# Kernel optimization log

Hardware: AMD Instinct MI355X
Metric: run time of the kernel (lower is better)

Reference implementation:

```python
import jax, jax.numpy as jnp
import numpy as np

EMBED_DIM = 1024
HEAD_DIM = 64


def setup_inputs() -> dict:
    key = jax.random.key(0)
    ks = jax.random.split(key, 7)
    s_in = EMBED_DIM ** -0.5  # torch Linear default init scale
    x = jax.random.normal(ks[0], (4, 4096, EMBED_DIM), dtype=jnp.float32)
    Wk = jax.random.uniform(ks[1], (HEAD_DIM, EMBED_DIM), jnp.float32, -s_in, s_in)
    bk = jax.random.uniform(ks[2], (HEAD_DIM,), jnp.float32, -s_in, s_in)
    Wq = jax.random.uniform(ks[3], (HEAD_DIM, EMBED_DIM), jnp.float32, -s_in, s_in)
    bq = jax.random.uniform(ks[4], (HEAD_DIM,), jnp.float32, -s_in, s_in)
    Wv = jax.random.uniform(ks[5], (HEAD_DIM, EMBED_DIM), jnp.float32, -s_in, s_in)
    bv = jax.random.uniform(ks[6], (HEAD_DIM,), jnp.float32, -s_in, s_in)
    return {"x": x, "Wq": Wq, "bq": bq, "Wk": Wk, "bk": bk, "Wv": Wv, "bv": bv}


def reference(x, Wq, bq, Wk, bk, Wv, bv):
    # torch Linear: y = x @ W.T + b
    q = jnp.einsum('btc,dc->btd', x, Wq) + bq  # [B,T,D]
    k = jnp.einsum('btc,dc->btd', x, Wk) + bk
    v = jnp.einsum('btc,dc->btd', x, Wv) + bv
    scale = HEAD_DIM ** -0.5
    # NOTE: original divides by scale (multiplies by sqrt(head_dim)) -- faithful
    scores = jnp.einsum('btd,bsd->bts', q, k) / scale  # [B,T,T]
    attn_weights = jax.nn.softmax(scores, axis=-1)
    return jnp.einsum('bts,bsd->btd', attn_weights, v)
```

## Files before the change

kernel.cpp:

```cpp
#include <hip/hip_runtime.h>

#define BATCH 4
#define SEQ   4096
#define CDIM  1024
#define DDIM  64
#define NROW  (BATCH * SEQ)
#define NSPL  8
#define KS    4
#define SEG   (NROW * DDIM)

typedef _Float16 f16;
typedef _Float16 f16x8 __attribute__((ext_vector_type(8)));
typedef _Float16 f16x4 __attribute__((ext_vector_type(4)));
typedef __fp16   h16x2 __attribute__((ext_vector_type(2)));
typedef float    f32x4 __attribute__((ext_vector_type(4)));

#define MFMA32(a, b, c) __builtin_amdgcn_mfma_f32_16x16x32_f16((a), (b), (c), 0, 0, 0)
#define MFMA16(a, b, c) __builtin_amdgcn_mfma_f32_16x16x16f16((a), (b), (c), 0, 0, 0)

#define GLDS(g, l)                                                            \
  __builtin_amdgcn_global_load_lds((const __attribute__((address_space(1))) void*)(g), \
                                   (__attribute__((address_space(3))) void*)(l), 16, 0, 0)

#define QSCALE 11.5415603f

__device__ inline f16x8 cvt8(f32x4 a, f32x4 b) {
  h16x2 p0 = __builtin_amdgcn_cvt_pkrtz(a[0], a[1]);
  h16x2 p1 = __builtin_amdgcn_cvt_pkrtz(a[2], a[3]);
  h16x2 p2 = __builtin_amdgcn_cvt_pkrtz(b[0], b[1]);
  h16x2 p3 = __builtin_amdgcn_cvt_pkrtz(b[2], b[3]);
  f16x8 r;
  r[0] = p0[0]; r[1] = p0[1]; r[2] = p1[0]; r[3] = p1[1];
  r[4] = p2[0]; r[5] = p2[1]; r[6] = p3[0]; r[7] = p3[1];
  return r;
}

__device__ inline f16x4 cvt4(float a, float b, float c, float d) {
  h16x2 lo = __builtin_amdgcn_cvt_pkrtz(a, b);
  h16x2 hi = __builtin_amdgcn_cvt_pkrtz(c, d);
  f16x4 r;
  r[0] = lo[0]; r[1] = lo[1]; r[2] = hi[0]; r[3] = hi[1];
  return r;
}

__global__ __launch_bounds__(256) void prep_w_kernel(const float* __restrict__ Wq,
                                                     const float* __restrict__ Wk,
                                                     const float* __restrict__ Wv,
                                                     f16* __restrict__ wf2) {
  const int t = blockIdx.x * 256 + threadIdx.x;
  const int lane = t & 63;
  const int s = t >> 6;
  const int mt = s % 12, ck = s / 12;
  const int mat = mt >> 2, tile = mt & 3;
  const int n = lane & 15, quad = lane >> 4;
  const float* W = (mat == 0) ? Wq : (mat == 1) ? Wk : Wv;
  const float* src = W + (size_t)(tile * 16 + n) * CDIM + ck * 32 + quad * 8;
  const f32x4 a = *(const f32x4*)src;
  const f32x4 b = *(const f32x4*)(src + 4);
  *(f16x8*)(wf2 + (size_t)t * 8) = cvt8(a, b);
}

__global__ __launch_bounds__(256, 4) void proj_kernel(const float* __restrict__ x,
                                                      const f16* __restrict__ wf2,
                                                      f16* __restrict__ ppart) {
  __shared__ __attribute__((aligned(16))) char smem[2][20480];
  const int tid = threadIdx.x, lane = tid & 63, w = tid >> 6;
  const int n = lane & 15, quad = lane >> 4;
  const int rw = w & 1, wc = w >> 1;
  const int rowblk = blockIdx.x >> 2, split = blockIdx.x & 3;
  const int rowbase = rowblk * 64;

  const float* xsrc[2];
#pragma unroll
  for (int j = 0; j < 2; ++j) {
    const int i = 2 * w + j;
    xsrc[j] = x + (size_t)(rowbase + i * 8 + (lane >> 3)) * CDIM + split * 256 + (lane & 7) * 4;
  }
  const f16* wsrc[3];
#pragma unroll
  for (int j = 0; j < 3; ++j) {
    const int mt = 3 * w + j;
    wsrc[j] = wf2 + (size_t)(split * 96 + mt) * 512 + lane * 8;
  }

  f32x4 acc[2][6];
#pragma unroll
  for (int rt = 0; rt < 2; ++rt)
#pragma unroll
    for (int i = 0; i < 6; ++i) acc[rt][i] = (f32x4){0.f, 0.f, 0.f, 0.f};

  auto issue = [&](int ck, int b) {
    char* base = &smem[b][0];
#pragma unroll
    for (int j = 0; j < 2; ++j)
      GLDS(xsrc[j] + ck * 32, base + (2 * w + j) * 1024);
#pragma unroll
    for (int j = 0; j < 3; ++j)
      GLDS(wsrc[j] + (size_t)ck * 6144, base + 8192 + (3 * w + j) * 1024);
  };

  issue(0, 0);
  for (int ck = 0; ck < 8; ++ck) {
    const int b = ck & 1;
    __syncthreads();
    if (ck + 1 < 8) issue(ck + 1, b ^ 1);
    const char* base = &smem[b][0];
    f16x8 a[2];
#pragma unroll
    for (int rt = 0; rt < 2; ++rt) {
      const int i = rw * 4 + rt * 2 + (n >> 3);
      const float* xp = (const float*)(base + i * 1024 + (n & 7) * 128 + quad * 32);
      a[rt] = cvt8(*(const f32x4*)xp, *(const f32x4*)(xp + 4));
    }
#pragma unroll
    for (int i2 = 0; i2 < 6; ++i2) {
      const f16x8 bf = *(const f16x8*)(base + 8192 + (wc * 6 + i2) * 1024 + lane * 16);
      acc[0][i2] = MFMA32(a[0], bf, acc[0][i2]);
      acc[1][i2] = MFMA32(a[1], bf, acc[1][i2]);
    }
  }

#pragma unroll
  for (int i2 = 0; i2 < 6; ++i2) {
    const int mt = wc * 6 + i2;
    const int mat = mt >> 2, tile = mt & 3;
    const int d = tile * 16 + n;
    f16* seg = ppart + ((size_t)mat * KS + split) * SEG;
#pragma unroll
    for (int rt = 0; rt < 2; ++rt) {
      const int r0 = rowbase + rw * 32 + rt * 16 + quad * 4;
      const f32x4 aa = acc[rt][i2];
      if (mat == 0) {
#pragma unroll
        for (int r = 0; r < 4; ++r)
          seg[(size_t)(r0 + r) * DDIM + d] = (f16)aa[r];
      } else if (mat == 1) {
#pragma unroll
        for (int r = 0; r < 4; ++r) {
          const int t = r0 + r;
          const int col = ((((d >> 3) ^ (t & 7)) << 3) | (d & 7));
          seg[(size_t)t * DDIM + col] = (f16)aa[r];
        }
      } else {
        const int bb = r0 >> 12;
        const int tl = r0 & (SEQ - 1);
        const int ck2 = tl >> 6;
        const int bsw = (((tl & 63) >> 2) ^ n) << 2;
        *(f16x4*)(seg + ((size_t)(bb * 64 + ck2) * 64 + d) * 64 + bsw) =
            cvt4(aa[0], aa[1], aa[2], aa[3]);
      }
    }
  }
}

__global__ __launch_bounds__(256) void combine_proj_kernel(const f16* __restrict__ ppart,
                                                           const float* __restrict__ bq,
                                                           const float* __restrict__ bk,
                                                           const float* __restrict__ bv,
                                                           f16* __restrict__ qs,
                                                           f16* __restrict__ ks,
                                                           f16* __restrict__ vc) {
  const int seg = blockIdx.x / 512;
  const int tix = (blockIdx.x - seg * 512) * 256 + threadIdx.x;
  const size_t base = (size_t)tix * 8;
  const f16* pp = ppart + (size_t)seg * KS * SEG + base;

  float s[8];
#pragma unroll
  for (int j = 0; j < 8; ++j) s[j] = 0.f;
#pragma unroll
  for (int sp = 0; sp < KS; ++sp) {
    const f16x8 v = *(const f16x8*)(pp + (size_t)sp * SEG);
#pragma unroll
    for (int j = 0; j < 8; ++j) s[j] += (float)v[j];
  }

  f16x8 o;
  if (seg == 0) {
    const int d0 = (int)(base & 63);
#pragma unroll
    for (int j = 0; j < 8; ++j) o[j] = (f16)((s[j] + bq[d0 + j]) * QSCALE);
    *(f16x8*)(qs + base) = o;
  } else if (seg == 1) {
    const int t = (int)(base >> 6);
    const int d0 = (((int)(base & 63) >> 3) ^ (t & 7)) << 3;
#pragma unroll
    for (int j = 0; j < 8; ++j) o[j] = (f16)(s[j] + bk[d0 + j]);
    *(f16x8*)(ks + base) = o;
  } else {
    const float b = bv[(int)(base >> 6) & 63];
#pragma unroll
    for (int j = 0; j < 8; ++j) o[j] = (f16)(s[j] + b);
    *(f16x8*)(vc + base) = o;
  }
}

template <int NSPLIT>
__global__ __launch_bounds__(256, 4) void attn_kernel(const f16* __restrict__ qs,
                                                      const f16* __restrict__ ks,
                                                      const f16* __restrict__ vc,
                                                      float* __restrict__ outp,
                                                      f16* __restrict__ pacc,
                                                      float* __restrict__ pm,
                                                      float* __restrict__ pl) {
  __shared__ __attribute__((aligned(16))) f16 lk[2][4096];
  __shared__ __attribute__((aligned(16))) f16 lv[2][4096];
  const int tid = threadIdx.x, lane = tid & 63, w = tid >> 6;
  const int n = lane & 15, quad = lane >> 4;
  const int split = blockIdx.x % NSPLIT;
  const int rowblk = blockIdx.x / NSPLIT;
  const int row0 = rowblk * 128 + w * 32;
  const int bb = row0 >> 12;
  const int kbase = split * (SEQ / NSPLIT);
  const int kc0 = kbase >> 6;
  const int NC = SEQ / NSPLIT / 64;

  const f16* ksb = ks + (size_t)bb * SEQ * DDIM;
  const f16* vcb = vc + (size_t)bb * 64 * 4096;

  auto issue = [&](int c, int buf) {
#pragma unroll
    for (int i = 0; i < 2; ++i) {
      const int id = 2 * w + i;
      GLDS(ksb + (size_t)(kbase + c * 64) * 64 + id * 512 + lane * 8, &lk[buf][id * 512]);
      GLDS(vcb + (size_t)(kc0 + c) * 4096 + id * 512 + lane * 8, &lv[buf][id * 512]);
    }
  };

  f16x8 qf[2][2];
#pragma unroll
  for (int g = 0; g < 2; ++g)
#pragma unroll
    for (int hh = 0; hh < 2; ++hh)
      qf[g][hh] = *(const f16x8*)(qs + (size_t)(row0 + g * 16 + n) * DDIM + hh * 32 + quad * 8);

  const int kswz = (quad ^ (n & 7)) << 3;
  int vswz[4];
#pragma unroll
  for (int st = 0; st < 4; ++st) vswz[st] = ((((st << 2) | quad) ^ n) << 2);

  f32x4 acc[2][4];
  float m[2] = {-1e30f, -1e30f}, ll[2] = {0.f, 0.f};
#pragma unroll
  for (int g = 0; g < 2; ++g)
#pragma unroll
    for (int t = 0; t < 4; ++t) acc[g][t] = (f32x4){0.f, 0.f, 0.f, 0.f};

  issue(0, 0);
  for (int c = 0; c < NC; ++c) {
    const int b = c & 1;
    __syncthreads();
    if (c + 1 < NC) issue(c + 1, b ^ 1);

    f32x4 s[2][4];
#pragma unroll
    for (int st = 0; st < 4; ++st) {
      const f16* lkr = &lk[b][(st * 16 + n) * 64];
      const f16x8 klo = *(const f16x8*)(lkr + kswz);
      const f16x8 khi = *(const f16x8*)(lkr + (kswz ^ 32));
#pragma unroll
      for (int g = 0; g < 2; ++g) {
        f32x4 z = (f32x4){0.f, 0.f, 0.f, 0.f};
        z = MFMA32(klo, qf[g][0], z);
        s[g][st] = MFMA32(khi, qf[g][1], z);
      }
    }

    f16x4 pq[2][4];
#pragma unroll
    for (int g = 0; g < 2; ++g) {
      f32x4 mx;
#pragma unroll
      for (int r = 0; r < 4; ++r)
        mx[r] = fmaxf(fmaxf(s[g][0][r], s[g][1][r]), fmaxf(s[g][2][r], s[g][3][r]));
      float mloc = fmaxf(fmaxf(mx[0], mx[1]), fmaxf(mx[2], mx[3]));
      mloc = fmaxf(mloc, __shfl_xor(mloc, 16));
      mloc = fmaxf(mloc, __shfl_xor(mloc, 32));
      const float mnew = fmaxf(m[g], mloc);
      const float alpha = __builtin_amdgcn_exp2f(m[g] - mnew);
      m[g] = mnew;
      float psum = 0.f;
#pragma unroll
      for (int st = 0; st < 4; ++st) {
        f32x4 p;
#pragma unroll
        for (int r = 0; r < 4; ++r) p[r] = __builtin_amdgcn_exp2f(s[g][st][r] - mnew);
        psum += (p[0] + p[1]) + (p[2] + p[3]);
        pq[g][st] = cvt4(p[0], p[1], p[2], p[3]);
      }
      ll[g] = ll[g] * alpha + psum;
#pragma unroll
      for (int t = 0; t < 4; ++t) acc[g][t] *= alpha;
    }

#pragma unroll
    for (int dt = 0; dt < 4; ++dt) {
      const f16* lvr = &lv[b][(dt * 16 + n) * 64];
#pragma unroll
      for (int st = 0; st < 4; ++st) {
        const f16x4 va = *(const f16x4*)(lvr + vswz[st]);
        acc[0][dt] = MFMA16(va, pq[0][st], acc[0][dt]);
        acc[1][dt] = MFMA16(va, pq[1][st], acc[1][dt]);
      }
    }
  }

  float lred[2];
#pragma unroll
  for (int g = 0; g < 2; ++g) {
    float l = ll[g];
    l += __shfl_xor(l, 16);
    l += __shfl_xor(l, 32);
    lred[g] = l;
  }

  if (NSPLIT == 1) {
#pragma unroll
    for (int g = 0; g < 2; ++g) {
      const float inv = 1.0f / lred[g];
      const int q = row0 + g * 16 + n;
#pragma unroll
      for (int t = 0; t < 4; ++t) {
        f32x4 o = acc[g][t];
#pragma unroll
        for (int r = 0; r < 4; ++r) o[r] *= inv;
        *(f32x4*)(outp + (size_t)q * DDIM + t * 16 + quad * 4) = o;
      }
    }
  } else {
#pragma unroll
    for (int g = 0; g < 2; ++g) {
      const int q = row0 + g * 16 + n;
#pragma unroll
      for (int t = 0; t < 4; ++t)
        *(f16x4*)(pacc + ((size_t)split * NROW + q) * DDIM + t * 16 + quad * 4) =
            cvt4(acc[g][t][0], acc[g][t][1], acc[g][t][2], acc[g][t][3]);
      if (quad == 0) {
        pm[split * NROW + q] = m[g];
        pl[split * NROW + q] = lred[g];
      }
    }
  }
}

template <int NSPLIT>
__global__ __launch_bounds__(256) void combine_kernel(const f16* __restrict__ pacc,
                                                      const float* __restrict__ pm,
                                                      const float* __restrict__ pl,
                                                      float* __restrict__ out) {
  const int idx = blockIdx.x * 256 + threadIdx.x;
  const int row = idx >> 4;
  const int c = (idx & 15) * 4;
  float mm = pm[row];
#pragma unroll
  for (int s = 1; s < NSPLIT; ++s) mm = fmaxf(mm, pm[s * NROW + row]);
  float L = 0.f;
  f32x4 o = (f32x4){0.f, 0.f, 0.f, 0.f};
#pragma unroll
  for (int s = 0; s < NSPLIT; ++s) {
    const float e = __builtin_amdgcn_exp2f(pm[s * NROW + row] - mm);
    L += pl[s * NROW + row] * e;
    const f16x4 a = *(const f16x4*)(pacc + ((size_t)s * NROW + row) * DDIM + c);
#pragma unroll
    for (int j = 0; j < 4; ++j) o[j] += (float)a[j] * e;
  }
  const float inv = 1.0f / L;
#pragma unroll
  for (int j = 0; j < 4; ++j) o[j] *= inv;
  *(f32x4*)(out + (size_t)row * DDIM + c) = o;
}

extern "C" void kernel_launch(void* const* d_in, const int* in_sizes, int n_in,
                              void* d_out, int out_size, void* d_ws, size_t ws_size,
                              hipStream_t stream) {
  const float* x  = (const float*)d_in[0];
  const float* Wq = (const float*)d_in[1];
  const float* bq = (const float*)d_in[2];
  const float* Wk = (const float*)d_in[3];
  const float* bk = (const float*)d_in[4];
  const float* Wv = (const float*)d_in[5];
  const float* bv = (const float*)d_in[6];
  float* out = (float*)d_out;

  f16* wf2 = (f16*)d_ws;
  f16* qs = wf2 + 3 * 65536;
  f16* ks = qs + (size_t)SEG;
  f16* vc = ks + (size_t)SEG;
  f16* ppart = vc + (size_t)SEG;
  f16* pacc = ppart + (size_t)3 * KS * SEG;
  float* pm = (float*)(pacc + (size_t)NSPL * SEG);
  float* pl = pm + (size_t)NSPL * NROW;
  const size_t need = (size_t)((char*)(pl + (size_t)NSPL * NROW) - (char*)d_ws);

  prep_w_kernel<<<dim3(96), dim3(256), 0, stream>>>(Wq, Wk, Wv, wf2);
  proj_kernel<<<dim3(256 * KS), dim3(256), 0, stream>>>(x, wf2, ppart);
  combine_proj_kernel<<<dim3(1536), dim3(256), 0, stream>>>(ppart, bq, bk, bv, qs, ks, vc);

  if (ws_size >= need) {
    attn_kernel<NSPL><<<dim3(128 * NSPL), dim3(256), 0, stream>>>(qs, ks, vc, nullptr, pacc, pm, pl);
    combine_kernel<NSPL><<<dim3(NROW * 16 / 256), dim3(256), 0, stream>>>(pacc, pm, pl, out);
  } else {
    attn_kernel<1><<<dim3(128), dim3(256), 0, stream>>>(qs, ks, vc, out, nullptr, nullptr, nullptr);
  }
}
```

Before: 158.1 us.

## Drop split-K in projection and fuse bias/combine into proj kernel

The projection kernel no longer splits the 1024-wide reduction into four partial fp16 buffers that a separate combine kernel sums. Each 512-thread block now handles 32 rows over the full reduction in 32 double-buffered steps and adds the bias and Q scale directly before writing Q, K and V. The x tile in shared memory uses an XOR swizzle to avoid bank conflicts. This removes one kernel launch and the write and reread of the partial buffers, but leaves fewer blocks and a longer serial reduction loop per block.

```diff
diff --git a/kernel.cpp b/kernel.cpp
--- a/kernel.cpp
+++ b/kernel.cpp
@@ -6,7 +6,6 @@
 #define DDIM  64
 #define NROW  (BATCH * SEQ)
 #define NSPL  8
-#define KS    4
 #define SEG   (NROW * DDIM)
 
 typedef _Float16 f16;
@@ -60,138 +59,101 @@
   *(f16x8*)(wf2 + (size_t)t * 8) = cvt8(a, b);
 }
 
-__global__ __launch_bounds__(256, 4) void proj_kernel(const float* __restrict__ x,
+__global__ __launch_bounds__(512, 4) void proj_kernel(const float* __restrict__ x,
                                                       const f16* __restrict__ wf2,
-                                                      f16* __restrict__ ppart) {
-  __shared__ __attribute__((aligned(16))) char smem[2][20480];
+                                                      const float* __restrict__ bq,
+                                                      const float* __restrict__ bk,
+                                                      const float* __restrict__ bv,
+                                                      f16* __restrict__ qs,
+                                                      f16* __restrict__ ks,
+                                                      f16* __restrict__ vc) {
+  __shared__ __attribute__((aligned(16))) char smem[2][16384];
   const int tid = threadIdx.x, lane = tid & 63, w = tid >> 6;
   const int n = lane & 15, quad = lane >> 4;
-  const int rw = w & 1, wc = w >> 1;
-  const int rowblk = blockIdx.x >> 2, split = blockIdx.x & 3;
-  const int rowbase = rowblk * 64;
-
-  const float* xsrc[2];
-#pragma unroll
-  for (int j = 0; j < 2; ++j) {
-    const int i = 2 * w + j;
-    xsrc[j] = x + (size_t)(rowbase + i * 8 + (lane >> 3)) * CDIM + split * 256 + (lane & 7) * 4;
-  }
-  const f16* wsrc[3];
-#pragma unroll
-  for (int j = 0; j < 3; ++j) {
-    const int mt = 3 * w + j;
-    wsrc[j] = wf2 + (size_t)(split * 96 + mt) * 512 + lane * 8;
-  }
-
-  f32x4 acc[2][6];
-#pragma unroll
-  for (int rt = 0; rt < 2; ++rt)
-#pragma unroll
-    for (int i = 0; i < 6; ++i) acc[rt][i] = (f32x4){0.f, 0.f, 0.f, 0.f};
+  const int rowbase = blockIdx.x * 32;
+
+  const float* xsrc[2] = {nullptr, nullptr};
+  const f16* wsrc[2] = {nullptr, nullptr};
+  int xdst[2] = {0, 0}, wdst[2] = {0, 0};
+  if (w < 2) {
+#pragma unroll
+    for (int j = 0; j < 2; ++j) {
+      const int i = 2 * w + j;
+      xsrc[j] = x + (size_t)(rowbase + i * 8 + (lane >> 3)) * CDIM +
+                (((lane & 7) ^ ((lane >> 3) & 7)) * 4);
+      xdst[j] = i * 1024;
+    }
+  } else {
+#pragma unroll
+    for (int j = 0; j < 2; ++j) {
+      const int mt = 2 * (w - 2) + j;
+      wsrc[j] = wf2 + (size_t)mt * 512 + lane * 8;
+      wdst[j] = 4096 + mt * 1024;
+    }
+  }
 
   auto issue = [&](int ck, int b) {
     char* base = &smem[b][0];
-#pragma unroll
-    for (int j = 0; j < 2; ++j)
-      GLDS(xsrc[j] + ck * 32, base + (2 * w + j) * 1024);
-#pragma unroll
-    for (int j = 0; j < 3; ++j)
-      GLDS(wsrc[j] + (size_t)ck * 6144, base + 8192 + (3 * w + j) * 1024);
+    if (w < 2) {
+#pragma unroll
+      for (int j = 0; j < 2; ++j) GLDS(xsrc[j] + ck * 32, base + xdst[j]);
+    } else {
+#pragma unroll
+      for (int j = 0; j < 2; ++j) GLDS(wsrc[j] + (size_t)ck * 6144, base + wdst[j]);
+    }
   };
 
+  const int rt = w >> 2, mtb = 3 * (w & 3);
+  f32x4 acc[3];
+#pragma unroll
+  for (int i = 0; i < 3; ++i) acc[i] = (f32x4){0.f, 0.f, 0.f, 0.f};
+
   issue(0, 0);
-  for (int ck = 0; ck < 8; ++ck) {
+  for (int ck = 0; ck < 32; ++ck) {
     const int b = ck & 1;
     __syncthreads();
-    if (ck + 1 < 8) issue(ck + 1, b ^ 1);
+    if (ck + 1 < 32) issue(ck + 1, b ^ 1);
     const char* base = &smem[b][0];
-    f16x8 a[2];
-#pragma unroll
-    for (int rt = 0; rt < 2; ++rt) {
-      const int i = rw * 4 + rt * 2 + (n >> 3);
-      const float* xp = (const float*)(base + i * 1024 + (n & 7) * 128 + quad * 32);
-      a[rt] = cvt8(*(const f32x4*)xp, *(const f32x4*)(xp + 4));
-    }
-#pragma unroll
-    for (int i2 = 0; i2 < 6; ++i2) {
-      const f16x8 bf = *(const f16x8*)(base + 8192 + (wc * 6 + i2) * 1024 + lane * 16);
-      acc[0][i2] = MFMA32(a[0], bf, acc[0][i2]);
-      acc[1][i2] = MFMA32(a[1], bf, acc[1][i2]);
-    }
-  }
-
-#pragma unroll
-  for (int i2 = 0; i2 < 6; ++i2) {
-    const int mt = wc * 6 + i2;
+    const char* xb = base + (rt * 16 + n) * 128;
+    const f32x4 xa = *(const f32x4*)(xb + ((((quad << 1) ^ (n & 7)) << 4)));
+    const f32x4 xc = *(const f32x4*)(xb + (((((quad << 1) | 1) ^ (n & 7)) << 4)));
+    const f16x8 a = cvt8(xa, xc);
+#pragma unroll
+    for (int i2 = 0; i2 < 3; ++i2) {
+      const f16x8 bf = *(const f16x8*)(base + 4096 + (mtb + i2) * 1024 + lane * 16);
+      acc[i2] = MFMA32(a, bf, acc[i2]);
+    }
+  }
+
+  const int r0 = rowbase + rt * 16 + quad * 4;
+#pragma unroll
+  for (int i2 = 0; i2 < 3; ++i2) {
+    const int mt = mtb + i2;
     const int mat = mt >> 2, tile = mt & 3;
     const int d = tile * 16 + n;
-    f16* seg = ppart + ((size_t)mat * KS + split) * SEG;
-#pragma unroll
-    for (int rt = 0; rt < 2; ++rt) {
-      const int r0 = rowbase + rw * 32 + rt * 16 + quad * 4;
-      const f32x4 aa = acc[rt][i2];
-      if (mat == 0) {
-#pragma unroll
-        for (int r = 0; r < 4; ++r)
-          seg[(size_t)(r0 + r) * DDIM + d] = (f16)aa[r];
-      } else if (mat == 1) {
-#pragma unroll
-        for (int r = 0; r < 4; ++r) {
-          const int t = r0 + r;
-          const int col = ((((d >> 3) ^ (t & 7)) << 3) | (d & 7));
-          seg[(size_t)t * DDIM + col] = (f16)aa[r];
-        }
-      } else {
-        const int bb = r0 >> 12;
-        const int tl = r0 & (SEQ - 1);
-        const int ck2 = tl >> 6;
-        const int bsw = (((tl & 63) >> 2) ^ n) << 2;
-        *(f16x4*)(seg + ((size_t)(bb * 64 + ck2) * 64 + d) * 64 + bsw) =
-            cvt4(aa[0], aa[1], aa[2], aa[3]);
-      }
-    }
-  }
-}
-
-__global__ __launch_bounds__(256) void combine_proj_kernel(const f16* __restrict__ ppart,
-                                                           const float* __restrict__ bq,
-                                                           const float* __restrict__ bk,
-                                                           const float* __restrict__ bv,
-                                                           f16* __restrict__ qs,
-                                                           f16* __restrict__ ks,
-                                                           f16* __restrict__ vc) {
-  const int seg = blockIdx.x / 512;
-  const int tix = (blockIdx.x - seg * 512) * 256 + threadIdx.x;
-  const size_t base = (size_t)tix * 8;
-  const f16* pp = ppart + (size_t)seg * KS * SEG + base;
-
-  float s[8];
-#pragma unroll
-  for (int j = 0; j < 8; ++j) s[j] = 0.f;
-#pragma unroll
-  for (int sp = 0; sp < KS; ++sp) {
-    const f16x8 v = *(const f16x8*)(pp + (size_t)sp * SEG);
-#pragma unroll
-    for (int j = 0; j < 8; ++j) s[j] += (float)v[j];
-  }
-
-  f16x8 o;
-  if (seg == 0) {
-    const int d0 = (int)(base & 63);
-#pragma unroll
-    for (int j = 0; j < 8; ++j) o[j] = (f16)((s[j] + bq[d0 + j]) * QSCALE);
-    *(f16x8*)(qs + base) = o;
-  } else if (seg == 1) {
-    const int t = (int)(base >> 6);
-    const int d0 = (((int)(base & 63) >> 3) ^ (t & 7)) << 3;
-#pragma unroll
-    for (int j = 0; j < 8; ++j) o[j] = (f16)(s[j] + bk[d0 + j]);
-    *(f16x8*)(ks + base) = o;
-  } else {
-    const float b = bv[(int)(base >> 6) & 63];
-#pragma unroll
-    for (int j = 0; j < 8; ++j) o[j] = (f16)(s[j] + b);
-    *(f16x8*)(vc + base) = o;
+    const f32x4 aa = acc[i2];
+    if (mat == 0) {
+      const float bi = bq[d];
+#pragma unroll
+      for (int r = 0; r < 4; ++r)
+        qs[(size_t)(r0 + r) * DDIM + d] = (f16)((aa[r] + bi) * QSCALE);
+    } else if (mat == 1) {
+      const float bi = bk[d];
+#pragma unroll
+      for (int r = 0; r < 4; ++r) {
+        const int t = r0 + r;
+        const int col = ((((d >> 3) ^ (t & 7)) << 3) | (d & 7));
+        ks[(size_t)t * DDIM + col] = (f16)(aa[r] + bi);
+      }
+    } else {
+      const float bi = bv[d];
+      const int bb = r0 >> 12;
+      const int tl = r0 & (SEQ - 1);
+      const int ck2 = tl >> 6;
+      const int bsw = (((tl & 63) >> 2) ^ n) << 2;
+      *(f16x4*)(vc + ((size_t)(bb * 64 + ck2) * 64 + d) * 64 + bsw) =
+          cvt4(aa[0] + bi, aa[1] + bi, aa[2] + bi, aa[3] + bi);
+    }
   }
 }
 
@@ -386,15 +348,13 @@
   f16* qs = wf2 + 3 * 65536;
   f16* ks = qs + (size_t)SEG;
   f16* vc = ks + (size_t)SEG;
-  f16* ppart = vc + (size_t)SEG;
-  f16* pacc = ppart + (size_t)3 * KS * SEG;
+  f16* pacc = vc + (size_t)SEG;
   float* pm = (float*)(pacc + (size_t)NSPL * SEG);
   float* pl = pm + (size_t)NSPL * NROW;
   const size_t need = (size_t)((char*)(pl + (size_t)NSPL * NROW) - (char*)d_ws);
 
   prep_w_kernel<<<dim3(96), dim3(256), 0, stream>>>(Wq, Wk, Wv, wf2);
-  proj_kernel<<<dim3(256 * KS), dim3(256), 0, stream>>>(x, wf2, ppart);
-  combine_proj_kernel<<<dim3(1536), dim3(256), 0, stream>>>(ppart, bq, bk, bv, qs, ks, vc);
+  proj_kernel<<<dim3(512), dim3(512), 0, stream>>>(x, wf2, bq, bk, bv, qs, ks, vc);
 
   if (ws_size >= need) {
     attn_kernel<NSPL><<<dim3(128 * NSPL), dim3(256), 0, stream>>>(qs, ks, vc, nullptr, pacc, pm, pl);
```

New measurement: 186.9 us. 18.2% more time.
